# Kernel tuning notes

Hardware: AMD Instinct MI355X
Metric: run time of the kernel (lower is better)

Reference implementation:

```python
import jax, jax.numpy as jnp
import numpy as np

B, P, H, N, D, K = 1024, 1024, 4096, 32, 512, 128


def setup_inputs() -> dict:
    key = jax.random.key(0)
    k1, k2, k3, k4, k5 = jax.random.split(key, 5)
    return {
        "proximal_input": jax.random.normal(k1, (B, P), dtype=jnp.float32),
        "distal_input": jax.random.normal(k2, (B, D), dtype=jnp.float32),
        "W": jax.random.normal(k3, (H, P), dtype=jnp.float32) / np.sqrt(P),
        "b": jax.random.normal(k4, (H,), dtype=jnp.float32) / np.sqrt(P),
        "distal": jax.random.normal(k5, (H, N, D), dtype=jnp.float32),
        "k": K,
    }


def reference(proximal_input, distal_input, W, b, distal, k):
    # proximal path: standard linear -> (B, H)
    proximal_output = proximal_input @ W.T + b
    # per-hidden-unit dendrite projections -> (H, B, N)
    distal_output = jnp.einsum('bd,hnd->hbn', distal_input, distal)
    # pick dominant dendrite by absolute value, keep its signed value
    abs_max_idx = jnp.argmax(jnp.abs(distal_output), axis=-1)          # (H, B)
    distal_max = jnp.take_along_axis(
        distal_output, abs_max_idx[..., None], axis=-1)[..., 0].T      # (B, H)
    # sigmoid gate modulates proximal activations
    result = proximal_output * jax.nn.sigmoid(distal_max)              # (B, H)
    # keep only top-k per row (scatter-built 0/1 mask, as in the original)
    _, top_idxs = jax.lax.top_k(result, k)                             # (B, k)
    rows = jnp.arange(result.shape[0])[:, None]
    mask = jnp.zeros_like(result).at[rows, top_idxs].set(1.0)
    return result * mask
```

## Files before the change

kernel.cpp:

```cpp
#include <hip/hip_runtime.h>
#include <cstdint>
#include <cmath>

#define Bsz  1024
#define Pdim 1024
#define Hdim 4096
#define Ndim 32
#define Ddim 512
#define Ktop 128

typedef _Float16 f16x8  __attribute__((ext_vector_type(8)));
typedef float    f32x16 __attribute__((ext_vector_type(16)));

#define GLDS(gsrc, ldst)                                                        \
  __builtin_amdgcn_global_load_lds(                                             \
      (const __attribute__((address_space(1))) unsigned int*)(gsrc),            \
      (__attribute__((address_space(3))) unsigned int*)(ldst), 16, 0, 0)

#define WS_NEEDED 270532608ull

__global__ __launch_bounds__(256) void convert_img(
    const float* __restrict__ src, char* __restrict__ dst, int kcbits)
{
  const int gid  = blockIdx.x * 256 + threadIdx.x;
  const int row  = gid >> kcbits;
  const int e    = (gid & ((1 << kcbits) - 1)) * 8;
  const int Krow = 8 << kcbits;
  float4 v0 = *(const float4*)(src + (size_t)row * Krow + e);
  float4 v1 = *(const float4*)(src + (size_t)row * Krow + e + 4);
  const int tile = row >> 7, r = row & 127, ks = e >> 5, k = e & 31;
  char* base = dst + (size_t)(tile * (Krow >> 5) + ks) * 16384;
  const int off = ((r >> 5) * 2 + (k >> 4)) * 1024
                + ((r & 31) + 32 * ((k >> 3) & 1)) * 16;
  const float f[8] = {v0.x, v0.y, v0.z, v0.w, v1.x, v1.y, v1.z, v1.w};
  f16x8 hi, lo;
#pragma unroll
  for (int j = 0; j < 8; j++) {
    const _Float16 h = (_Float16)f[j];
    hi[j] = h;
    lo[j] = (_Float16)((f[j] - (float)h) * 256.f);
  }
  *(f16x8*)(base + off)        = hi;
  *(f16x8*)(base + 8192 + off) = lo;
}

__global__ __launch_bounds__(256, 2) void proximal_mfma(
    const char* __restrict__ Aw, const char* __restrict__ Bw,
    const float* __restrict__ bias, float* __restrict__ out)
{
  __shared__ __align__(16) char lds[2][32768];
  const int t = threadIdx.x, lane = t & 63, wv = t >> 6;
  const int hi32 = lane >> 5, c31 = lane & 31;
  const int wrow0 = (wv >> 1) * 64, wcol0 = (wv & 1) * 64;

  const int blk = blockIdx.x;
  const int xcd = blk & 7, q = blk >> 3;
  const int htile = xcd * 4 + (q >> 3);
  const int btile = q & 7;
  const int h0 = htile * 128, b0 = btile * 128;

  f32x16 acc[2][2], accx[2][2];
#pragma unroll
  for (int mi = 0; mi < 2; mi++)
#pragma unroll
    for (int ni = 0; ni < 2; ni++) {
      acc[mi][ni]  = (f32x16)(0.f);
      accx[mi][ni] = (f32x16)(0.f);
    }

  const char* Abase = Aw + (size_t)(htile * 32) * 16384;
  const char* Bbase = Bw + (size_t)(btile * 32) * 16384;

  auto STAGE = [&](char* bufp, int ks) {
    const char* As = Abase + ks * 16384;
    const char* Bs = Bbase + ks * 16384;
#pragma unroll
    for (int j = 0; j < 4; j++) {
      const int ch = j * 4 + wv;
      GLDS(As + ch * 1024 + lane * 16, bufp + ch * 1024);
      GLDS(Bs + ch * 1024 + lane * 16, bufp + 16384 + ch * 1024);
    }
  };

  STAGE(lds[0], 0);
  __syncthreads();

  int cur = 0;
  for (int ks = 0; ks < 32; ++ks) {
    if (ks < 31) STAGE(lds[cur ^ 1], ks + 1);

    const char* L = lds[cur];
    f16x8 ah[2][2], al[2][2];
#pragma unroll
    for (int mi = 0; mi < 2; mi++)
#pragma unroll
      for (int kk = 0; kk < 2; kk++) {
        const int fa = ((wrow0 >> 5) + mi) * 2 + kk;
        ah[mi][kk] = *(const f16x8*)(L + fa * 1024 + lane * 16);
        al[mi][kk] = *(const f16x8*)(L + 8192 + fa * 1024 + lane * 16);
      }
    __builtin_amdgcn_s_setprio(1);
#pragma unroll
    for (int ni = 0; ni < 2; ni++) {
      f16x8 bh[2], bl[2];
#pragma unroll
      for (int kk = 0; kk < 2; kk++) {
        const int fb = ((wcol0 >> 5) + ni) * 2 + kk;
        bh[kk] = *(const f16x8*)(L + 16384 + fb * 1024 + lane * 16);
        bl[kk] = *(const f16x8*)(L + 24576 + fb * 1024 + lane * 16);
      }
#pragma unroll
      for (int mi = 0; mi < 2; mi++)
#pragma unroll
        for (int kk = 0; kk < 2; kk++) {
          acc[mi][ni]  = __builtin_amdgcn_mfma_f32_32x32x16_f16(ah[mi][kk], bh[kk], acc[mi][ni],  0, 0, 0);
          accx[mi][ni] = __builtin_amdgcn_mfma_f32_32x32x16_f16(ah[mi][kk], bl[kk], accx[mi][ni], 0, 0, 0);
          accx[mi][ni] = __builtin_amdgcn_mfma_f32_32x32x16_f16(al[mi][kk], bh[kk], accx[mi][ni], 0, 0, 0);
        }
    }
    __builtin_amdgcn_s_setprio(0);
    __syncthreads();
    cur ^= 1;
  }

#pragma unroll
  for (int mi = 0; mi < 2; ++mi)
#pragma unroll
    for (int ni = 0; ni < 2; ++ni) {
      const int bcol = b0 + wcol0 + ni * 32 + c31;
#pragma unroll
      for (int qq = 0; qq < 4; ++qq) {
        const int hb = h0 + wrow0 + mi * 32 + qq * 8 + hi32 * 4;
        const float4 bb = *(const float4*)(bias + hb);
        float4 o;
        o.x = acc[mi][ni][4*qq+0] + accx[mi][ni][4*qq+0] * 0.00390625f + bb.x;
        o.y = acc[mi][ni][4*qq+1] + accx[mi][ni][4*qq+1] * 0.00390625f + bb.y;
        o.z = acc[mi][ni][4*qq+2] + accx[mi][ni][4*qq+2] * 0.00390625f + bb.z;
        o.w = acc[mi][ni][4*qq+3] + accx[mi][ni][4*qq+3] * 0.00390625f + bb.w;
        *(float4*)(out + (size_t)bcol * Hdim + hb) = o;
      }
    }
}

__global__ __launch_bounds__(256, 2) void distal_mfma(
    const char* __restrict__ Aw, const char* __restrict__ Bw,
    float* __restrict__ out)
{
  __shared__ __align__(16) char lds[2][32768];
  const int t = threadIdx.x, lane = t & 63, wv = t >> 6;
  const int hi32 = lane >> 5, c31 = lane & 31;
  const int wrow0 = (wv >> 1) * 64, wcol0 = (wv & 1) * 64;

  const int blk = blockIdx.x;
  const int xcd = blk & 7, q = blk >> 3;
  const int ntile = xcd * 128 + (q >> 3);
  const int btile = q & 7;

  f32x16 acc[2][2], accx[2][2];
#pragma unroll
  for (int mi = 0; mi < 2; mi++)
#pragma unroll
    for (int ni = 0; ni < 2; ni++) {
      acc[mi][ni]  = (f32x16)(0.f);
      accx[mi][ni] = (f32x16)(0.f);
    }

  const char* Abase = Aw + (size_t)(ntile * 16) * 16384;
  const char* Bbase = Bw + (size_t)(btile * 16) * 16384;

  auto STAGE = [&](char* bufp, int ks) {
    const char* As = Abase + ks * 16384;
    const char* Bs = Bbase + ks * 16384;
#pragma unroll
    for (int j = 0; j < 4; j++) {
      const int ch = j * 4 + wv;
      GLDS(As + ch * 1024 + lane * 16, bufp + ch * 1024);
      GLDS(Bs + ch * 1024 + lane * 16, bufp + 16384 + ch * 1024);
    }
  };

  STAGE(lds[0], 0);
  __syncthreads();

  int cur = 0;
  for (int ks = 0; ks < 16; ++ks) {
    if (ks < 15) STAGE(lds[cur ^ 1], ks + 1);

    const char* L = lds[cur];
    f16x8 ah[2][2], al[2][2];
#pragma unroll
    for (int mi = 0; mi < 2; mi++)
#pragma unroll
      for (int kk = 0; kk < 2; kk++) {
        const int fa = ((wrow0 >> 5) + mi) * 2 + kk;
        ah[mi][kk] = *(const f16x8*)(L + fa * 1024 + lane * 16);
        al[mi][kk] = *(const f16x8*)(L + 8192 + fa * 1024 + lane * 16);
      }
    __builtin_amdgcn_s_setprio(1);
#pragma unroll
    for (int ni = 0; ni < 2; ni++) {
      f16x8 bh[2], bl[2];
#pragma unroll
      for (int kk = 0; kk < 2; kk++) {
        const int fb = ((wcol0 >> 5) + ni) * 2 + kk;
        bh[kk] = *(const f16x8*)(L + 16384 + fb * 1024 + lane * 16);
        bl[kk] = *(const f16x8*)(L + 24576 + fb * 1024 + lane * 16);
      }
#pragma unroll
      for (int mi = 0; mi < 2; mi++)
#pragma unroll
        for (int kk = 0; kk < 2; kk++) {
          acc[mi][ni]  = __builtin_amdgcn_mfma_f32_32x32x16_f16(ah[mi][kk], bh[kk], acc[mi][ni],  0, 0, 0);
          accx[mi][ni] = __builtin_amdgcn_mfma_f32_32x32x16_f16(ah[mi][kk], bl[kk], accx[mi][ni], 0, 0, 0);
          accx[mi][ni] = __builtin_amdgcn_mfma_f32_32x32x16_f16(al[mi][kk], bh[kk], accx[mi][ni], 0, 0, 0);
        }
    }
    __builtin_amdgcn_s_setprio(0);
    __syncthreads();
    cur ^= 1;
  }

#pragma unroll
  for (int mi = 0; mi < 2; ++mi)
#pragma unroll
    for (int ni = 0; ni < 2; ++ni) {
      float bestA = -1.f, bestV = 0.f;
      int   bestN = 999;
#pragma unroll
      for (int reg = 0; reg < 16; ++reg) {
        const float v = acc[mi][ni][reg] + accx[mi][ni][reg] * 0.00390625f;
        const float a = fabsf(v);
        const int   n = (reg & 3) + 8 * (reg >> 2) + 4 * hi32;
        if (a > bestA) { bestA = a; bestV = v; bestN = n; }
      }
      {
        const float oa = __shfl_xor(bestA, 32, 64);
        const float ov = __shfl_xor(bestV, 32, 64);
        const int   on = __shfl_xor(bestN, 32, 64);
        if (oa > bestA || (oa == bestA && on < bestN)) {
          bestA = oa; bestV = ov; bestN = on;
        }
      }
      if (hi32 == 0) {
        const int bcol = btile * 128 + wcol0 + ni * 32 + c31;
        const int h    = ntile * 4 + (wrow0 >> 5) + mi;
        const float gate = 1.f / (1.f + expf(-bestV));
        out[(size_t)bcol * Hdim + h] *= gate;
      }
    }
}

__global__ __launch_bounds__(256) void proximal_gemm(
    const float* __restrict__ pin, const float* __restrict__ W,
    const float* __restrict__ bias, float* __restrict__ out)
{
  __shared__ float Blds[32 * 256];
  __shared__ float Alds[32 * 32];
  const int t  = threadIdx.x;
  const int l  = t & 63;
  const int wv = t >> 6;
  const int ell   = blockIdx.x;
  const int xcd   = ell & 7;
  const int q     = ell >> 3;
  const int htile = xcd * 2 + (q >> 5);
  const int btile = q & 31;
  const int h0 = htile * 256, b0 = btile * 32;

  float acc[8][4];
#pragma unroll
  for (int i = 0; i < 8; i++)
    for (int j = 0; j < 4; j++) acc[i][j] = 0.f;

  const float* wrow = W + (size_t)(h0 + t) * Pdim;
  const int ab = t >> 3, ak = (t & 7) * 4;
  const float* arow = pin + (size_t)(b0 + ab) * Pdim + ak;

  for (int kt = 0; kt < Pdim / 32; ++kt) {
    const int p0 = kt * 32;
    float wbuf[32];
#pragma unroll
    for (int f = 0; f < 8; f++) {
      float4 v = *(const float4*)(wrow + p0 + f * 4);
      wbuf[f * 4 + 0] = v.x; wbuf[f * 4 + 1] = v.y;
      wbuf[f * 4 + 2] = v.z; wbuf[f * 4 + 3] = v.w;
    }
    float4 av = *(const float4*)(arow + p0);
    __syncthreads();
#pragma unroll
    for (int f = 0; f < 32; f++) Blds[f * 256 + t] = wbuf[f];
    Alds[(ak + 0) * 32 + ab] = av.x;
    Alds[(ak + 1) * 32 + ab] = av.y;
    Alds[(ak + 2) * 32 + ab] = av.z;
    Alds[(ak + 3) * 32 + ab] = av.w;
    __syncthreads();
#pragma unroll
    for (int k = 0; k < 32; k++) {
      float4 bv  = *(const float4*)&Blds[k * 256 + 4 * l];
      float4 alo = *(const float4*)&Alds[k * 32 + 8 * wv];
      float4 ahi = *(const float4*)&Alds[k * 32 + 8 * wv + 4];
      float a0[8] = {alo.x, alo.y, alo.z, alo.w, ahi.x, ahi.y, ahi.z, ahi.w};
#pragma unroll
      for (int i = 0; i < 8; i++) {
        acc[i][0] += a0[i] * bv.x;
        acc[i][1] += a0[i] * bv.y;
        acc[i][2] += a0[i] * bv.z;
        acc[i][3] += a0[i] * bv.w;
      }
    }
  }
  float4 bb = *(const float4*)(bias + h0 + 4 * l);
#pragma unroll
  for (int i = 0; i < 8; i++) {
    float4 o;
    o.x = acc[i][0] + bb.x;
    o.y = acc[i][1] + bb.y;
    o.z = acc[i][2] + bb.z;
    o.w = acc[i][3] + bb.w;
    *(float4*)(out + (size_t)(b0 + 8 * wv + i) * Hdim + h0 + 4 * l) = o;
  }
}

__global__ __launch_bounds__(256) void distal_gate_fb(
    const float* __restrict__ din, const float* __restrict__ distal,
    float* __restrict__ out)
{
  __shared__ float Blds[32 * 256];
  __shared__ float Alds[32 * 32];
  const int t  = threadIdx.x;
  const int l  = t & 63;
  const int wv = t >> 6;
  const int ell   = blockIdx.x;
  const int xcd   = ell & 7;
  const int q     = ell >> 3;
  const int htile = xcd * 64 + (q >> 5);
  const int btile = q & 31;
  const int n0 = htile * 256, b0 = btile * 32;

  float acc[8][4];
#pragma unroll
  for (int i = 0; i < 8; i++)
    for (int j = 0; j < 4; j++) acc[i][j] = 0.f;

  const float* brow = distal + (size_t)(n0 + t) * Ddim;
  const int ab = t >> 3, ak = (t & 7) * 4;
  const float* arow = din + (size_t)(b0 + ab) * Ddim + ak;

  for (int kt = 0; kt < Ddim / 32; ++kt) {
    const int d0 = kt * 32;
    float wbuf[32];
#pragma unroll
    for (int f = 0; f < 8; f++) {
      float4 v = *(const float4*)(brow + d0 + f * 4);
      wbuf[f * 4 + 0] = v.x; wbuf[f * 4 + 1] = v.y;
      wbuf[f * 4 + 2] = v.z; wbuf[f * 4 + 3] = v.w;
    }
    float4 av = *(const float4*)(arow + d0);
    __syncthreads();
#pragma unroll
    for (int f = 0; f < 32; f++) Blds[f * 256 + t] = wbuf[f];
    Alds[(ak + 0) * 32 + ab] = av.x;
    Alds[(ak + 1) * 32 + ab] = av.y;
    Alds[(ak + 2) * 32 + ab] = av.z;
    Alds[(ak + 3) * 32 + ab] = av.w;
    __syncthreads();
#pragma unroll
    for (int k = 0; k < 32; k++) {
      float4 bv  = *(const float4*)&Blds[k * 256 + 4 * l];
      float4 alo = *(const float4*)&Alds[k * 32 + 8 * wv];
      float4 ahi = *(const float4*)&Alds[k * 32 + 8 * wv + 4];
      float a0[8] = {alo.x, alo.y, alo.z, alo.w, ahi.x, ahi.y, ahi.z, ahi.w};
#pragma unroll
      for (int i = 0; i < 8; i++) {
        acc[i][0] += a0[i] * bv.x;
        acc[i][1] += a0[i] * bv.y;
        acc[i][2] += a0[i] * bv.z;
        acc[i][3] += a0[i] * bv.w;
      }
    }
  }
  const int i0  = l & 7;
  const int grp = l >> 3;
  float v = 0.f;
#pragma unroll
  for (int bi = 0; bi < 8; bi++) {
    float bav = fabsf(acc[bi][0]);
    float bv_ = acc[bi][0];
    int   bn  = 4 * i0;
#pragma unroll
    for (int j = 1; j < 4; j++) {
      float av2 = fabsf(acc[bi][j]);
      if (av2 > bav) { bav = av2; bv_ = acc[bi][j]; bn = 4 * i0 + j; }
    }
#pragma unroll
    for (int m = 1; m < 8; m <<= 1) {
      float oav = __shfl_xor(bav, m, 64);
      float ov  = __shfl_xor(bv_, m, 64);
      int   on  = __shfl_xor(bn,  m, 64);
      if (oav > bav || (oav == bav && on < bn)) { bav = oav; bv_ = ov; bn = on; }
    }
    if (bi == i0) v = bv_;
  }
  const float gate = 1.f / (1.f + expf(-v));
  const size_t idx = (size_t)(b0 + 8 * wv + i0) * Hdim + (size_t)htile * 8 + grp;
  out[idx] *= gate;
}

__device__ __forceinline__ unsigned keyf(float f) {
  unsigned u = __float_as_uint(f);
  return (u & 0x80000000u) ? ~u : (u | 0x80000000u);
}

__global__ __launch_bounds__(256) void topk_mask(float* __restrict__ out)
{
  __shared__ float vals[Hdim];
  __shared__ unsigned hist[256];
  __shared__ unsigned sc[4];
  __shared__ unsigned s_prefix, s_kk;
  const int t = threadIdx.x;
  float* row = out + (size_t)blockIdx.x * Hdim;

#pragma unroll
  for (int qq = 0; qq < 4; qq++) {
    float4 v = *(const float4*)(row + qq * 1024 + t * 4);
    *(float4*)&vals[qq * 1024 + t * 4] = v;
  }
  if (t == 0) { s_prefix = 0u; s_kk = Ktop; }
  __syncthreads();

  for (int shift = 24; shift >= 0; shift -= 8) {
    hist[t] = 0u;
    __syncthreads();
    const unsigned prefix = s_prefix;
    const unsigned maskhi = (shift == 24) ? 0u : (0xFFFFFFFFu << (shift + 8));
    for (int c = 0; c < 16; c++) {
      unsigned u = keyf(vals[c * 256 + t]);
      if ((u & maskhi) == prefix)
        atomicAdd(&hist[(u >> shift) & 255u], 1u);
    }
    __syncthreads();
    if (t == 0) {
      unsigned kk = s_kk, cum = 0;
      int bin = 255;
      for (; bin > 0; --bin) {
        unsigned c = hist[bin];
        if (cum + c >= kk) break;
        cum += c;
      }
      s_kk = kk - cum;
      s_prefix = prefix | ((unsigned)bin << shift);
    }
    __syncthreads();
  }
  const unsigned T  = s_prefix;
  const unsigned kk = s_kk;

  const int lane = t & 63, w = t >> 6;
  unsigned running = 0;
  for (int c = 0; c < 16; c++) {
    const int h = c * 256 + t;
    const float v = vals[h];
    const unsigned u = keyf(v);
    const bool tie = (u == T);
    unsigned long long m = __ballot(tie);
    unsigned lpfx = (unsigned)__popcll(m & ((1ull << lane) - 1ull));
    if (lane == 0) sc[w] = (unsigned)__popcll(m);
    __syncthreads();
    unsigned off = 0;
#pragma unroll
    for (int ww = 0; ww < 4; ww++) if (ww < w) off += sc[ww];
    const unsigned rank = running + off + lpfx;
    row[h] = (u > T) ? v : ((tie && rank < kk) ? v : 0.f);
    const unsigned tot = sc[0] + sc[1] + sc[2] + sc[3];
    __syncthreads();
    running += tot;
  }
}

extern "C" void kernel_launch(void* const* d_in, const int* in_sizes, int n_in,
                              void* d_out, int out_size, void* d_ws, size_t ws_size,
                              hipStream_t stream)
{
  (void)in_sizes; (void)n_in; (void)out_size;
  const float* pin  = (const float*)d_in[0];
  const float* dinp = (const float*)d_in[1];
  const float* W    = (const float*)d_in[2];
  const float* bias = (const float*)d_in[3];
  const float* dst  = (const float*)d_in[4];
  float* out = (float*)d_out;

  if (ws_size >= WS_NEEDED) {
    char* ws = (char*)d_ws;
    hipLaunchKernelGGL(convert_img,   dim3(2048),  dim3(256), 0, stream, W,   ws,             7);
    hipLaunchKernelGGL(convert_img,   dim3(512),   dim3(256), 0, stream, pin, ws + 16777216,  7);
    hipLaunchKernelGGL(proximal_mfma, dim3(256),   dim3(256), 0, stream, ws, ws + 16777216, bias, out);
    hipLaunchKernelGGL(convert_img,   dim3(32768), dim3(256), 0, stream, dst,  ws,             6);
    hipLaunchKernelGGL(convert_img,   dim3(256),   dim3(256), 0, stream, dinp, ws + 268435456, 6);
    hipLaunchKernelGGL(distal_mfma,   dim3(8192),  dim3(256), 0, stream, ws, ws + 268435456, out);
  } else {
    hipLaunchKernelGGL(proximal_gemm, dim3(512),   dim3(256), 0, stream, pin, W, bias, out);
    hipLaunchKernelGGL(distal_gate_fb, dim3(16384), dim3(256), 0, stream, dinp, dst, out);
  }

  hipLaunchKernelGGL(topk_mask, dim3(Bsz), dim3(256), 0, stream, out);
}
```

Before: 623.5 us.

## Switch MFMA GEMM loops to 4-buffer half-K pipeline with explicit vmcnt waits

Both fp16-split MFMA GEMM kernels now stage half-K-step slices into a 4-deep ring of 16KB LDS buffers. Loads run two stages ahead, and each iteration waits with a partial s_waitcnt vmcnt plus a single barrier, where it used to do a full syncthreads after every 32-wide K step. The aim is to keep more global-to-LDS traffic in flight and take barrier stalls off the MFMA path. In exchange there are twice as many iterations and barriers, and correctness now depends on hand-counted vmcnt values and on ring-buffer reuse being safe with only one barrier per stage.

```diff
diff --git a/kernel.cpp b/kernel.cpp
--- a/kernel.cpp
+++ b/kernel.cpp
@@ -44,14 +44,54 @@
   *(f16x8*)(base + 8192 + off) = lo;
 }
 
+#define PIPE_LOOP(NH)                                                           \
+  STAGE(0);                                                                     \
+  STAGE(1);                                                                     \
+  for (int h = 0; h < (NH); ++h) {                                              \
+    if (h + 2 < (NH)) {                                                         \
+      STAGE(h + 2);                                                             \
+      asm volatile("s_waitcnt vmcnt(8)" ::: "memory");                          \
+    } else if (h + 1 < (NH)) {                                                  \
+      asm volatile("s_waitcnt vmcnt(4)" ::: "memory");                          \
+    } else {                                                                    \
+      asm volatile("s_waitcnt vmcnt(0)" ::: "memory");                          \
+    }                                                                           \
+    __builtin_amdgcn_s_barrier();                                               \
+    asm volatile("" ::: "memory");                                              \
+    const char* buf = lds[h & 3];                                               \
+    f16x8 ah[2], al[2], bh[2], bl[2];                                           \
+    _Pragma("unroll")                                                           \
+    for (int mi = 0; mi < 2; mi++) {                                            \
+      const int m = wr * 2 + mi;                                                \
+      ah[mi] = *(const f16x8*)(buf + m * 1024 + lane * 16);                     \
+      al[mi] = *(const f16x8*)(buf + 4096 + m * 1024 + lane * 16);              \
+    }                                                                           \
+    _Pragma("unroll")                                                           \
+    for (int ni = 0; ni < 2; ni++) {                                            \
+      const int m = wc * 2 + ni;                                                \
+      bh[ni] = *(const f16x8*)(buf + 8192 + m * 1024 + lane * 16);              \
+      bl[ni] = *(const f16x8*)(buf + 12288 + m * 1024 + lane * 16);             \
+    }                                                                           \
+    __builtin_amdgcn_s_setprio(1);                                              \
+    _Pragma("unroll")                                                           \
+    for (int ni = 0; ni < 2; ni++)                                              \
+      _Pragma("unroll")                                                         \
+      for (int mi = 0; mi < 2; mi++) {                                          \
+        acc[mi][ni]  = __builtin_amdgcn_mfma_f32_32x32x16_f16(ah[mi], bh[ni], acc[mi][ni],  0, 0, 0); \
+        accx[mi][ni] = __builtin_amdgcn_mfma_f32_32x32x16_f16(ah[mi], bl[ni], accx[mi][ni], 0, 0, 0); \
+        accx[mi][ni] = __builtin_amdgcn_mfma_f32_32x32x16_f16(al[mi], bh[ni], accx[mi][ni], 0, 0, 0); \
+      }                                                                         \
+    __builtin_amdgcn_s_setprio(0);                                              \
+  }
+
 __global__ __launch_bounds__(256, 2) void proximal_mfma(
     const char* __restrict__ Aw, const char* __restrict__ Bw,
     const float* __restrict__ bias, float* __restrict__ out)
 {
-  __shared__ __align__(16) char lds[2][32768];
+  __shared__ __align__(16) char lds[4][16384];
   const int t = threadIdx.x, lane = t & 63, wv = t >> 6;
   const int hi32 = lane >> 5, c31 = lane & 31;
-  const int wrow0 = (wv >> 1) * 64, wcol0 = (wv & 1) * 64;
+  const int wr = wv >> 1, wc = wv & 1;
 
   const int blk = blockIdx.x;
   const int xcd = blk & 7, q = blk >> 3;
@@ -71,66 +111,30 @@
   const char* Abase = Aw + (size_t)(htile * 32) * 16384;
   const char* Bbase = Bw + (size_t)(btile * 32) * 16384;
 
-  auto STAGE = [&](char* bufp, int ks) {
-    const char* As = Abase + ks * 16384;
-    const char* Bs = Bbase + ks * 16384;
+  auto STAGE = [&](int h) {
+    const int ks = h >> 1, kk = h & 1;
+    char* buf = lds[h & 3];
+    const char* Ai = Abase + (size_t)ks * 16384;
+    const char* Bi = Bbase + (size_t)ks * 16384;
+    const char* srcs[4] = {Ai, Ai + 8192, Bi, Bi + 8192};
 #pragma unroll
     for (int j = 0; j < 4; j++) {
-      const int ch = j * 4 + wv;
-      GLDS(As + ch * 1024 + lane * 16, bufp + ch * 1024);
-      GLDS(Bs + ch * 1024 + lane * 16, bufp + 16384 + ch * 1024);
+      const int c = j * 4 + wv;
+      GLDS(srcs[j] + (wv * 2 + kk) * 1024 + lane * 16,
+           buf + c * 1024 + lane * 16);
     }
   };
 
-  STAGE(lds[0], 0);
-  __syncthreads();
-
-  int cur = 0;
-  for (int ks = 0; ks < 32; ++ks) {
-    if (ks < 31) STAGE(lds[cur ^ 1], ks + 1);
-
-    const char* L = lds[cur];
-    f16x8 ah[2][2], al[2][2];
-#pragma unroll
-    for (int mi = 0; mi < 2; mi++)
-#pragma unroll
-      for (int kk = 0; kk < 2; kk++) {
-        const int fa = ((wrow0 >> 5) + mi) * 2 + kk;
-        ah[mi][kk] = *(const f16x8*)(L + fa * 1024 + lane * 16);
-        al[mi][kk] = *(const f16x8*)(L + 8192 + fa * 1024 + lane * 16);
-      }
-    __builtin_amdgcn_s_setprio(1);
-#pragma unroll
-    for (int ni = 0; ni < 2; ni++) {
-      f16x8 bh[2], bl[2];
-#pragma unroll
-      for (int kk = 0; kk < 2; kk++) {
-        const int fb = ((wcol0 >> 5) + ni) * 2 + kk;
-        bh[kk] = *(const f16x8*)(L + 16384 + fb * 1024 + lane * 16);
-        bl[kk] = *(const f16x8*)(L + 24576 + fb * 1024 + lane * 16);
-      }
-#pragma unroll
-      for (int mi = 0; mi < 2; mi++)
-#pragma unroll
-        for (int kk = 0; kk < 2; kk++) {
-          acc[mi][ni]  = __builtin_amdgcn_mfma_f32_32x32x16_f16(ah[mi][kk], bh[kk], acc[mi][ni],  0, 0, 0);
-          accx[mi][ni] = __builtin_amdgcn_mfma_f32_32x32x16_f16(ah[mi][kk], bl[kk], accx[mi][ni], 0, 0, 0);
-          accx[mi][ni] = __builtin_amdgcn_mfma_f32_32x32x16_f16(al[mi][kk], bh[kk], accx[mi][ni], 0, 0, 0);
-        }
-    }
-    __builtin_amdgcn_s_setprio(0);
-    __syncthreads();
-    cur ^= 1;
-  }
+  PIPE_LOOP(64)
 
 #pragma unroll
   for (int mi = 0; mi < 2; ++mi)
 #pragma unroll
     for (int ni = 0; ni < 2; ++ni) {
-      const int bcol = b0 + wcol0 + ni * 32 + c31;
+      const int bcol = b0 + wc * 64 + ni * 32 + c31;
 #pragma unroll
       for (int qq = 0; qq < 4; ++qq) {
-        const int hb = h0 + wrow0 + mi * 32 + qq * 8 + hi32 * 4;
+        const int hb = h0 + wr * 64 + mi * 32 + qq * 8 + hi32 * 4;
         const float4 bb = *(const float4*)(bias + hb);
         float4 o;
         o.x = acc[mi][ni][4*qq+0] + accx[mi][ni][4*qq+0] * 0.00390625f + bb.x;
@@ -146,10 +150,10 @@
     const char* __restrict__ Aw, const char* __restrict__ Bw,
     float* __restrict__ out)
 {
-  __shared__ __align__(16) char lds[2][32768];
+  __shared__ __align__(16) char lds[4][16384];
   const int t = threadIdx.x, lane = t & 63, wv = t >> 6;
   const int hi32 = lane >> 5, c31 = lane & 31;
-  const int wrow0 = (wv >> 1) * 64, wcol0 = (wv & 1) * 64;
+  const int wr = wv >> 1, wc = wv & 1;
 
   const int blk = blockIdx.x;
   const int xcd = blk & 7, q = blk >> 3;
@@ -168,57 +172,21 @@
   const char* Abase = Aw + (size_t)(ntile * 16) * 16384;
   const char* Bbase = Bw + (size_t)(btile * 16) * 16384;
 
-  auto STAGE = [&](char* bufp, int ks) {
-    const char* As = Abase + ks * 16384;
-    const char* Bs = Bbase + ks * 16384;
+  auto STAGE = [&](int h) {
+    const int ks = h >> 1, kk = h & 1;
+    char* buf = lds[h & 3];
+    const char* Ai = Abase + (size_t)ks * 16384;
+    const char* Bi = Bbase + (size_t)ks * 16384;
+    const char* srcs[4] = {Ai, Ai + 8192, Bi, Bi + 8192};
 #pragma unroll
     for (int j = 0; j < 4; j++) {
-      const int ch = j * 4 + wv;
-      GLDS(As + ch * 1024 + lane * 16, bufp + ch * 1024);
-      GLDS(Bs + ch * 1024 + lane * 16, bufp + 16384 + ch * 1024);
+      const int c = j * 4 + wv;
+      GLDS(srcs[j] + (wv * 2 + kk) * 1024 + lane * 16,
+           buf + c * 1024 + lane * 16);
     }
   };
 
-  STAGE(lds[0], 0);
-  __syncthreads();
-
-  int cur = 0;
-  for (int ks = 0; ks < 16; ++ks) {
-    if (ks < 15) STAGE(lds[cur ^ 1], ks + 1);
-
-    const char* L = lds[cur];
-    f16x8 ah[2][2], al[2][2];
-#pragma unroll
-    for (int mi = 0; mi < 2; mi++)
-#pragma unroll
-      for (int kk = 0; kk < 2; kk++) {
-        const int fa = ((wrow0 >> 5) + mi) * 2 + kk;
-        ah[mi][kk] = *(const f16x8*)(L + fa * 1024 + lane * 16);
-        al[mi][kk] = *(const f16x8*)(L + 8192 + fa * 1024 + lane * 16);
-      }
-    __builtin_amdgcn_s_setprio(1);
-#pragma unroll
-    for (int ni = 0; ni < 2; ni++) {
-      f16x8 bh[2], bl[2];
-#pragma unroll
-      for (int kk = 0; kk < 2; kk++) {
-        const int fb = ((wcol0 >> 5) + ni) * 2 + kk;
-        bh[kk] = *(const f16x8*)(L + 16384 + fb * 1024 + lane * 16);
-        bl[kk] = *(const f16x8*)(L + 24576 + fb * 1024 + lane * 16);
-      }
-#pragma unroll
-      for (int mi = 0; mi < 2; mi++)
-#pragma unroll
-        for (int kk = 0; kk < 2; kk++) {
-          acc[mi][ni]  = __builtin_amdgcn_mfma_f32_32x32x16_f16(ah[mi][kk], bh[kk], acc[mi][ni],  0, 0, 0);
-          accx[mi][ni] = __builtin_amdgcn_mfma_f32_32x32x16_f16(ah[mi][kk], bl[kk], accx[mi][ni], 0, 0, 0);
-          accx[mi][ni] = __builtin_amdgcn_mfma_f32_32x32x16_f16(al[mi][kk], bh[kk], accx[mi][ni], 0, 0, 0);
-        }
-    }
-    __builtin_amdgcn_s_setprio(0);
-    __syncthreads();
-    cur ^= 1;
-  }
+  PIPE_LOOP(32)
 
 #pragma unroll
   for (int mi = 0; mi < 2; ++mi)
@@ -242,8 +210,8 @@
         }
       }
       if (hi32 == 0) {
-        const int bcol = btile * 128 + wcol0 + ni * 32 + c31;
-        const int h    = ntile * 4 + (wrow0 >> 5) + mi;
+        const int bcol = btile * 128 + wc * 64 + ni * 32 + c31;
+        const int h    = ntile * 4 + wr * 2 + mi;
         const float gate = 1.f / (1.f + expf(-bestV));
         out[(size_t)bcol * Hdim + h] *= gate;
       }
```

Result: no change. 615.1 us (-1.3%).
